# Performance work log

Hardware: AMD Instinct MI355X
Metric: run time of the kernel (lower is better)

Reference implementation:

```python
import jax, jax.numpy as jnp
import numpy as np

B, D, H, E, K = 16384, 4096, 2048, 64, 2
TEMPERATURE = 0.8  # training=True


def setup_inputs() -> dict:
    key = jax.random.key(0)
    k1, k2, k3 = jax.random.split(key, 3)
    x = jax.random.normal(k1, (B, D), dtype=jnp.float32)
    W1 = jax.random.normal(k2, (H, D), dtype=jnp.float32) * 0.02
    b1 = jnp.zeros((H,), dtype=jnp.float32)
    W2 = jax.random.normal(k3, (E, H), dtype=jnp.float32) * 0.02
    b2 = jnp.zeros((E,), dtype=jnp.float32)
    return {"x": x, "W1": W1, "b1": b1, "W2": W2, "b2": b2}


def reference(x, W1, b1, W2, b2):
    # router MLP: Linear(D->H) -> ReLU -> Linear(H->E)
    h = jax.nn.relu(jnp.einsum('bd,hd->bh', x, W1) + b1)
    router_logits = jnp.einsum('bh,eh->be', h, W2) + b2  # [B, E]

    # temperature-scaled softmax for routing
    routing_probs = jax.nn.softmax(router_logits / TEMPERATURE, axis=1)
    routing_weights, expert_indices = jax.lax.top_k(routing_probs, K)  # [B, K]
    routing_weights = routing_weights / routing_weights.sum(axis=1, keepdims=True)

    # entropy-based uncertainty uses UN-scaled logits
    full_probs = jax.nn.softmax(router_logits, axis=1)
    entropy = -jnp.sum(full_probs * jnp.log(full_probs + 1e-10), axis=1).mean()
    uncertainty = entropy / jnp.log(jnp.float32(E))
    return routing_weights, expert_indices, uncertainty
```

## Files before the change

### kernel.cpp

```cpp
#include <hip/hip_runtime.h>
#include <hip/hip_bf16.h>
#include <math.h>

#define B_ROWS 16384
#define D_DIM  4096
#define H_DIM  2048
#define E_DIM  64
#define TEMP   0.8f

typedef __bf16 bf16x8 __attribute__((ext_vector_type(8)));
typedef float  f32x4  __attribute__((ext_vector_type(4)));
typedef unsigned short ushort8 __attribute__((ext_vector_type(8)));

__device__ __forceinline__ unsigned short bf_rne(float f) {
  unsigned u = __float_as_uint(f);
  u += 0x7FFF + ((u >> 16) & 1);
  return (unsigned short)(u >> 16);
}

__device__ __forceinline__ void async_copy16(const void* g, void* l) {
  __builtin_amdgcn_global_load_lds(
      (const __attribute__((address_space(1))) void*)g,
      (__attribute__((address_space(3))) void*)l, 16, 0, 0);
}

__global__ __launch_bounds__(256) void split_kernel(
    const float* __restrict__ in, unsigned short* __restrict__ hi,
    unsigned short* __restrict__ lo) {
  const size_t i = ((size_t)blockIdx.x * 256 + threadIdx.x) * 8;
  float4 v0 = *(const float4*)(in + i);
  float4 v1 = *(const float4*)(in + i + 4);
  float f[8] = {v0.x, v0.y, v0.z, v0.w, v1.x, v1.y, v1.z, v1.w};
  ushort8 hv, lv;
#pragma unroll
  for (int j = 0; j < 8; ++j) {
    unsigned short h = bf_rne(f[j]);
    float fh = __uint_as_float(((unsigned)h) << 16);
    hv[j] = h;
    lv[j] = bf_rne(f[j] - fh);
  }
  *(ushort8*)(hi + i) = hv;
  *(ushort8*)(lo + i) = lv;
}

#define BM 128
#define BN 128
#define BKK 32

__global__ __launch_bounds__(256) void gemm1_mfma_kernel(
    const float* __restrict__ x,
    const unsigned short* __restrict__ w1h,
    const unsigned short* __restrict__ w1l,
    const float* __restrict__ b1, float* __restrict__ Hout) {
  __shared__ unsigned short Ah[BM * BKK];
  __shared__ unsigned short Al[BM * BKK];
  __shared__ unsigned short Bh[BN * BKK];
  __shared__ unsigned short Bl[BN * BKK];

  const int t    = threadIdx.x;
  const int lane = t & 63;
  const int w    = t >> 6;
  const int wm   = w >> 1;
  const int wn   = w & 1;
  const int m0   = blockIdx.y * BM;
  const int n0   = blockIdx.x * BN;

  const int e0 = (w * 2 + 0) * 512 + lane * 8;
  const int e1 = (w * 2 + 1) * 512 + lane * 8;
  const int r0 = e0 >> 5, c0 = e0 & 31;
  const int r1 = e1 >> 5, c1 = e1 & 31;
  const unsigned short* bh_g0 = w1h + (size_t)(n0 + r0) * D_DIM + c0;
  const unsigned short* bh_g1 = w1h + (size_t)(n0 + r1) * D_DIM + c1;
  const unsigned short* bl_g0 = w1l + (size_t)(n0 + r0) * D_DIM + c0;
  const unsigned short* bl_g1 = w1l + (size_t)(n0 + r1) * D_DIM + c1;
  unsigned short* bh_l0 = &Bh[e0];
  unsigned short* bh_l1 = &Bh[e1];
  unsigned short* bl_l0 = &Bl[e0];
  unsigned short* bl_l1 = &Bl[e1];

  const int ar = t >> 1;
  const int ac = (t & 1) * 16;
  const float* xp = x + (size_t)(m0 + ar) * D_DIM + ac;
  unsigned short* ah_w = &Ah[ar * BKK + ac];
  unsigned short* al_w = &Al[ar * BKK + ac];

  const int koff = (lane >> 4) * 8;
  const unsigned short* a_rd[4];
  const unsigned short* b_rd[4];
#pragma unroll
  for (int f = 0; f < 4; ++f) {
    a_rd[f] = &Ah[(wm * 64 + f * 16 + (lane & 15)) * BKK + koff];
    b_rd[f] = &Bh[(wn * 64 + f * 16 + (lane & 15)) * BKK + koff];
  }
  const int lo_off_a = (int)(Al - Ah);
  const int lo_off_b = (int)(Bl - Bh);

  f32x4 acc[4][4];
#pragma unroll
  for (int i = 0; i < 4; ++i)
#pragma unroll
    for (int j = 0; j < 4; ++j) acc[i][j] = (f32x4)0.f;

  for (int k0 = 0; k0 < D_DIM; k0 += BKK) {
    async_copy16(bh_g0 + k0, bh_l0);
    async_copy16(bh_g1 + k0, bh_l1);
    async_copy16(bl_g0 + k0, bl_l0);
    async_copy16(bl_g1 + k0, bl_l1);

    float4 v[4];
#pragma unroll
    for (int j = 0; j < 4; ++j) v[j] = *(const float4*)(xp + k0 + j * 4);
    float f[16] = {v[0].x, v[0].y, v[0].z, v[0].w, v[1].x, v[1].y, v[1].z, v[1].w,
                   v[2].x, v[2].y, v[2].z, v[2].w, v[3].x, v[3].y, v[3].z, v[3].w};
    ushort8 hv0, hv1, lv0, lv1;
#pragma unroll
    for (int j = 0; j < 8; ++j) {
      unsigned short h = bf_rne(f[j]);
      float fh = __uint_as_float(((unsigned)h) << 16);
      hv0[j] = h;
      lv0[j] = bf_rne(f[j] - fh);
    }
#pragma unroll
    for (int j = 0; j < 8; ++j) {
      unsigned short h = bf_rne(f[8 + j]);
      float fh = __uint_as_float(((unsigned)h) << 16);
      hv1[j] = h;
      lv1[j] = bf_rne(f[8 + j] - fh);
    }
    *(ushort8*)(ah_w)     = hv0;
    *(ushort8*)(ah_w + 8) = hv1;
    *(ushort8*)(al_w)     = lv0;
    *(ushort8*)(al_w + 8) = lv1;

    __syncthreads();

    bf16x8 fa_h[4], fa_l[4], fb_h[4], fb_l[4];
#pragma unroll
    for (int ff = 0; ff < 4; ++ff) {
      fa_h[ff] = *(const bf16x8*)(a_rd[ff]);
      fa_l[ff] = *(const bf16x8*)(a_rd[ff] + lo_off_a);
      fb_h[ff] = *(const bf16x8*)(b_rd[ff]);
      fb_l[ff] = *(const bf16x8*)(b_rd[ff] + lo_off_b);
    }
#pragma unroll
    for (int i = 0; i < 4; ++i)
#pragma unroll
      for (int j = 0; j < 4; ++j) {
        acc[i][j] = __builtin_amdgcn_mfma_f32_16x16x32_bf16(fa_h[i], fb_h[j], acc[i][j], 0, 0, 0);
        acc[i][j] = __builtin_amdgcn_mfma_f32_16x16x32_bf16(fa_l[i], fb_h[j], acc[i][j], 0, 0, 0);
        acc[i][j] = __builtin_amdgcn_mfma_f32_16x16x32_bf16(fa_h[i], fb_l[j], acc[i][j], 0, 0, 0);
      }
    __syncthreads();
  }

#pragma unroll
  for (int fn = 0; fn < 4; ++fn) {
    const int n = n0 + wn * 64 + fn * 16 + (lane & 15);
    const float bias = b1[n];
#pragma unroll
    for (int fm = 0; fm < 4; ++fm) {
      const int mbase = m0 + wm * 64 + fm * 16 + (lane >> 4) * 4;
#pragma unroll
      for (int r = 0; r < 4; ++r) {
        float vv = acc[fm][fn][r] + bias;
        Hout[(size_t)(mbase + r) * H_DIM + n] = fmaxf(vv, 0.f);
      }
    }
  }
}

#define F_BM 64
#define F_BK 32

__global__ __launch_bounds__(256) void gemm2_router_kernel(
    const float* __restrict__ h,
    const unsigned short* __restrict__ w2h,
    const unsigned short* __restrict__ w2l,
    const float* __restrict__ b2,
    float* __restrict__ out, float* __restrict__ accum) {
  __shared__ unsigned short Ah[F_BM * F_BK];
  __shared__ unsigned short Al[F_BM * F_BK];
  __shared__ unsigned short Bh[E_DIM * F_BK];
  __shared__ unsigned short Bl[E_DIM * F_BK];
  __shared__ float LG[F_BM][E_DIM + 1];

  const int t    = threadIdx.x;
  const int lane = t & 63;
  const int w    = t >> 6;
  const int m0   = blockIdx.x * F_BM;

  const int ar = t >> 2;
  const int ac = (t & 3) * 8;
  const float* hp = h + (size_t)(m0 + ar) * H_DIM + ac;
  unsigned short* ah_w = &Ah[ar * F_BK + ac];
  unsigned short* al_w = &Al[ar * F_BK + ac];

  const unsigned short* bh_g = w2h + (size_t)ar * H_DIM + ac;
  const unsigned short* bl_g = w2l + (size_t)ar * H_DIM + ac;
  unsigned short* bh_l = &Bh[t * 8];
  unsigned short* bl_l = &Bl[t * 8];

  const int koff = (lane >> 4) * 8;
  const unsigned short* a_rd = &Ah[(w * 16 + (lane & 15)) * F_BK + koff];
  const unsigned short* b_rd[4];
#pragma unroll
  for (int f = 0; f < 4; ++f)
    b_rd[f] = &Bh[(f * 16 + (lane & 15)) * F_BK + koff];
  const int lo_off_a = (int)(Al - Ah);
  const int lo_off_b = (int)(Bl - Bh);

  f32x4 acc[4];
#pragma unroll
  for (int f = 0; f < 4; ++f) acc[f] = (f32x4)0.f;

  for (int k0 = 0; k0 < H_DIM; k0 += F_BK) {
    async_copy16(bh_g + k0, bh_l);
    async_copy16(bl_g + k0, bl_l);

    float4 v0 = *(const float4*)(hp + k0);
    float4 v1 = *(const float4*)(hp + k0 + 4);
    float f[8] = {v0.x, v0.y, v0.z, v0.w, v1.x, v1.y, v1.z, v1.w};
    ushort8 hv, lv;
#pragma unroll
    for (int j = 0; j < 8; ++j) {
      unsigned short hh = bf_rne(f[j]);
      float fh = __uint_as_float(((unsigned)hh) << 16);
      hv[j] = hh;
      lv[j] = bf_rne(f[j] - fh);
    }
    *(ushort8*)ah_w = hv;
    *(ushort8*)al_w = lv;

    __syncthreads();

    bf16x8 fa_h = *(const bf16x8*)(a_rd);
    bf16x8 fa_l = *(const bf16x8*)(a_rd + lo_off_a);
#pragma unroll
    for (int f = 0; f < 4; ++f) {
      bf16x8 fb_h = *(const bf16x8*)(b_rd[f]);
      bf16x8 fb_l = *(const bf16x8*)(b_rd[f] + lo_off_b);
      acc[f] = __builtin_amdgcn_mfma_f32_16x16x32_bf16(fa_h, fb_h, acc[f], 0, 0, 0);
      acc[f] = __builtin_amdgcn_mfma_f32_16x16x32_bf16(fa_l, fb_h, acc[f], 0, 0, 0);
      acc[f] = __builtin_amdgcn_mfma_f32_16x16x32_bf16(fa_h, fb_l, acc[f], 0, 0, 0);
    }
    __syncthreads();
  }

#pragma unroll
  for (int f = 0; f < 4; ++f) {
    const int e = f * 16 + (lane & 15);
    const float bias = b2[e];
#pragma unroll
    for (int r = 0; r < 4; ++r) {
      const int ml = w * 16 + (lane >> 4) * 4 + r;
      LG[ml][e] = acc[f][r] + bias;
    }
  }
  __syncthreads();

  if (t < F_BM) {
    const int row = m0 + t;
    float l0 = LG[t][0]; int i0 = 0;
    float l1 = -INFINITY; int i1 = -1;
#pragma unroll
    for (int e = 1; e < E_DIM; ++e) {
      float v = LG[t][e];
      if (v > l0)      { l1 = l0; i1 = i0; l0 = v; i0 = e; }
      else if (v > l1) { l1 = v; i1 = e; }
    }

    const float eT = expf((l1 - l0) / TEMP);
    const float w0 = 1.f / (1.f + eT);
    const float w1 = eT / (1.f + eT);

    float Z = 0.f;
#pragma unroll
    for (int e = 0; e < E_DIM; ++e) Z += expf(LG[t][e] - l0);
    const float invZ = 1.f / Z;
    float ent = 0.f;
#pragma unroll
    for (int e = 0; e < E_DIM; ++e) {
      float p = expf(LG[t][e] - l0) * invZ;
      ent -= p * logf(p + 1e-10f);
    }

    out[(size_t)row * 2 + 0] = w0;
    out[(size_t)row * 2 + 1] = w1;
    out[(size_t)B_ROWS * 2 + (size_t)row * 2 + 0] = (float)i0;
    out[(size_t)B_ROWS * 2 + (size_t)row * 2 + 1] = (float)i1;

#pragma unroll
    for (int off = 32; off > 0; off >>= 1) ent += __shfl_down(ent, off);
    if (t == 0) atomicAdd(accum, ent);
  }
}

__global__ void zero_kernel(float* p) { p[0] = 0.f; }

__global__ void finalize_kernel(const float* __restrict__ accum,
                                float* __restrict__ out) {
  out[(size_t)B_ROWS * 4] = accum[0] / ((float)B_ROWS * logf((float)E_DIM));
}

extern "C" void kernel_launch(void* const* d_in, const int* in_sizes, int n_in,
                              void* d_out, int out_size, void* d_ws,
                              size_t ws_size, hipStream_t stream) {
  const float* x  = (const float*)d_in[0];
  const float* W1 = (const float*)d_in[1];
  const float* b1 = (const float*)d_in[2];
  const float* W2 = (const float*)d_in[3];
  const float* b2 = (const float*)d_in[4];
  float* out = (float*)d_out;

  unsigned short* w1h = (unsigned short*)d_ws;
  unsigned short* w1l = w1h + (size_t)H_DIM * D_DIM;
  unsigned short* w2h = w1l + (size_t)H_DIM * D_DIM;
  unsigned short* w2l = w2h + (size_t)E_DIM * H_DIM;
  float* h     = (float*)(w2l + (size_t)E_DIM * H_DIM);
  float* accum = h + (size_t)B_ROWS * H_DIM;

  zero_kernel<<<1, 1, 0, stream>>>(accum);

  split_kernel<<<(H_DIM * D_DIM) / (256 * 8), 256, 0, stream>>>(W1, w1h, w1l);
  split_kernel<<<(E_DIM * H_DIM) / (256 * 8), 256, 0, stream>>>(W2, w2h, w2l);

  dim3 g1(H_DIM / BN, B_ROWS / BM);
  gemm1_mfma_kernel<<<g1, 256, 0, stream>>>(x, w1h, w1l, b1, h);

  gemm2_router_kernel<<<B_ROWS / F_BM, 256, 0, stream>>>(h, w2h, w2l, b2, out, accum);

  finalize_kernel<<<1, 1, 0, stream>>>(accum, out);
}
```

Baseline: 1.278 ms.

## Use 32x32 MFMA tiles in GEMM1, deepen and prefetch GEMM2, fold zero kernel

GEMM1 switches from 16x16x32 to 32x32x16 bf16 MFMA instructions with 2x2 fragments per wave, which cuts the LDS fragment reads per MFMA and uses the larger-tile instruction. GEMM2 doubles its K tile to 64 and register-prefetches the next h tile across the barrier, so global latency overlaps with compute and fewer barriers are needed. The accumulator zeroing moves into the W2 split kernel, removing one launch. The costs are higher register pressure from the 16-wide accumulators and more LDS in GEMM2.

```diff
diff --git a/kernel.cpp b/kernel.cpp
--- a/kernel.cpp
+++ b/kernel.cpp
@@ -10,6 +10,7 @@
 
 typedef __bf16 bf16x8 __attribute__((ext_vector_type(8)));
 typedef float  f32x4  __attribute__((ext_vector_type(4)));
+typedef float  f32x16 __attribute__((ext_vector_type(16)));
 typedef unsigned short ushort8 __attribute__((ext_vector_type(8)));
 
 __device__ __forceinline__ unsigned short bf_rne(float f) {
@@ -26,7 +27,8 @@
 
 __global__ __launch_bounds__(256) void split_kernel(
     const float* __restrict__ in, unsigned short* __restrict__ hi,
-    unsigned short* __restrict__ lo) {
+    unsigned short* __restrict__ lo, float* zp) {
+  if (zp && blockIdx.x == 0 && threadIdx.x == 0) *zp = 0.f;
   const size_t i = ((size_t)blockIdx.x * 256 + threadIdx.x) * 8;
   float4 v0 = *(const float4*)(in + i);
   float4 v1 = *(const float4*)(in + i + 4);
@@ -84,22 +86,22 @@
   unsigned short* ah_w = &Ah[ar * BKK + ac];
   unsigned short* al_w = &Al[ar * BKK + ac];
 
-  const int koff = (lane >> 4) * 8;
-  const unsigned short* a_rd[4];
-  const unsigned short* b_rd[4];
-#pragma unroll
-  for (int f = 0; f < 4; ++f) {
-    a_rd[f] = &Ah[(wm * 64 + f * 16 + (lane & 15)) * BKK + koff];
-    b_rd[f] = &Bh[(wn * 64 + f * 16 + (lane & 15)) * BKK + koff];
+  const int koff = (lane >> 5) * 8;
+  const unsigned short* a_rd[2];
+  const unsigned short* b_rd[2];
+#pragma unroll
+  for (int f = 0; f < 2; ++f) {
+    a_rd[f] = &Ah[(wm * 64 + f * 32 + (lane & 31)) * BKK + koff];
+    b_rd[f] = &Bh[(wn * 64 + f * 32 + (lane & 31)) * BKK + koff];
   }
   const int lo_off_a = (int)(Al - Ah);
   const int lo_off_b = (int)(Bl - Bh);
 
-  f32x4 acc[4][4];
-#pragma unroll
-  for (int i = 0; i < 4; ++i)
-#pragma unroll
-    for (int j = 0; j < 4; ++j) acc[i][j] = (f32x4)0.f;
+  f32x16 acc[2][2];
+#pragma unroll
+  for (int i = 0; i < 2; ++i)
+#pragma unroll
+    for (int j = 0; j < 2; ++j) acc[i][j] = (f32x16)0.f;
 
   for (int k0 = 0; k0 < D_DIM; k0 += BKK) {
     async_copy16(bh_g0 + k0, bh_l0);
@@ -134,43 +136,48 @@
 
     __syncthreads();
 
-    bf16x8 fa_h[4], fa_l[4], fb_h[4], fb_l[4];
-#pragma unroll
-    for (int ff = 0; ff < 4; ++ff) {
-      fa_h[ff] = *(const bf16x8*)(a_rd[ff]);
-      fa_l[ff] = *(const bf16x8*)(a_rd[ff] + lo_off_a);
-      fb_h[ff] = *(const bf16x8*)(b_rd[ff]);
-      fb_l[ff] = *(const bf16x8*)(b_rd[ff] + lo_off_b);
-    }
-#pragma unroll
-    for (int i = 0; i < 4; ++i)
-#pragma unroll
-      for (int j = 0; j < 4; ++j) {
-        acc[i][j] = __builtin_amdgcn_mfma_f32_16x16x32_bf16(fa_h[i], fb_h[j], acc[i][j], 0, 0, 0);
-        acc[i][j] = __builtin_amdgcn_mfma_f32_16x16x32_bf16(fa_l[i], fb_h[j], acc[i][j], 0, 0, 0);
-        acc[i][j] = __builtin_amdgcn_mfma_f32_16x16x32_bf16(fa_h[i], fb_l[j], acc[i][j], 0, 0, 0);
+#pragma unroll
+    for (int ks = 0; ks < 2; ++ks) {
+      const int ko = ks * 16;
+      bf16x8 fa_h[2], fa_l[2], fb_h[2], fb_l[2];
+#pragma unroll
+      for (int ff = 0; ff < 2; ++ff) {
+        fa_h[ff] = *(const bf16x8*)(a_rd[ff] + ko);
+        fa_l[ff] = *(const bf16x8*)(a_rd[ff] + ko + lo_off_a);
+        fb_h[ff] = *(const bf16x8*)(b_rd[ff] + ko);
+        fb_l[ff] = *(const bf16x8*)(b_rd[ff] + ko + lo_off_b);
       }
+#pragma unroll
+      for (int i = 0; i < 2; ++i)
+#pragma unroll
+        for (int j = 0; j < 2; ++j) {
+          acc[i][j] = __builtin_amdgcn_mfma_f32_32x32x16_bf16(fa_h[i], fb_h[j], acc[i][j], 0, 0, 0);
+          acc[i][j] = __builtin_amdgcn_mfma_f32_32x32x16_bf16(fa_l[i], fb_h[j], acc[i][j], 0, 0, 0);
+          acc[i][j] = __builtin_amdgcn_mfma_f32_32x32x16_bf16(fa_h[i], fb_l[j], acc[i][j], 0, 0, 0);
+        }
+    }
     __syncthreads();
   }
 
 #pragma unroll
-  for (int fn = 0; fn < 4; ++fn) {
-    const int n = n0 + wn * 64 + fn * 16 + (lane & 15);
+  for (int fn = 0; fn < 2; ++fn) {
+    const int n = n0 + wn * 64 + fn * 32 + (lane & 31);
     const float bias = b1[n];
 #pragma unroll
-    for (int fm = 0; fm < 4; ++fm) {
-      const int mbase = m0 + wm * 64 + fm * 16 + (lane >> 4) * 4;
-#pragma unroll
-      for (int r = 0; r < 4; ++r) {
-        float vv = acc[fm][fn][r] + bias;
-        Hout[(size_t)(mbase + r) * H_DIM + n] = fmaxf(vv, 0.f);
+    for (int fm = 0; fm < 2; ++fm) {
+      const int mbase = m0 + wm * 64 + fm * 32 + 4 * (lane >> 5);
+#pragma unroll
+      for (int reg = 0; reg < 16; ++reg) {
+        const int row = mbase + (reg & 3) + 8 * (reg >> 2);
+        float vv = acc[fm][fn][reg] + bias;
+        Hout[(size_t)row * H_DIM + n] = fmaxf(vv, 0.f);
       }
     }
   }
 }
 
 #define F_BM 64
-#define F_BK 32
+#define F_BK 64
 
 __global__ __launch_bounds__(256) void gemm2_router_kernel(
     const float* __restrict__ h,
@@ -190,15 +197,23 @@
   const int m0   = blockIdx.x * F_BM;
 
   const int ar = t >> 2;
-  const int ac = (t & 3) * 8;
+  const int ac = (t & 3) * 16;
   const float* hp = h + (size_t)(m0 + ar) * H_DIM + ac;
   unsigned short* ah_w = &Ah[ar * F_BK + ac];
   unsigned short* al_w = &Al[ar * F_BK + ac];
 
-  const unsigned short* bh_g = w2h + (size_t)ar * H_DIM + ac;
-  const unsigned short* bl_g = w2l + (size_t)ar * H_DIM + ac;
-  unsigned short* bh_l = &Bh[t * 8];
-  unsigned short* bl_l = &Bl[t * 8];
+  const int e0 = (w * 2 + 0) * 512 + lane * 8;
+  const int e1 = (w * 2 + 1) * 512 + lane * 8;
+  const int r0 = e0 >> 6, c0 = e0 & 63;
+  const int r1 = e1 >> 6, c1 = e1 & 63;
+  const unsigned short* bh_g0 = w2h + (size_t)r0 * H_DIM + c0;
+  const unsigned short* bh_g1 = w2h + (size_t)r1 * H_DIM + c1;
+  const unsigned short* bl_g0 = w2l + (size_t)r0 * H_DIM + c0;
+  const unsigned short* bl_g1 = w2l + (size_t)r1 * H_DIM + c1;
+  unsigned short* bh_l0 = &Bh[e0];
+  unsigned short* bh_l1 = &Bh[e1];
+  unsigned short* bl_l0 = &Bl[e0];
+  unsigned short* bl_l1 = &Bl[e1];
 
   const int koff = (lane >> 4) * 8;
   const unsigned short* a_rd = &Ah[(w * 16 + (lane & 15)) * F_BK + koff];
@@ -213,35 +228,62 @@
 #pragma unroll
   for (int f = 0; f < 4; ++f) acc[f] = (f32x4)0.f;
 
+  float4 p0 = *(const float4*)(hp);
+  float4 p1 = *(const float4*)(hp + 4);
+  float4 p2 = *(const float4*)(hp + 8);
+  float4 p3 = *(const float4*)(hp + 12);
+
   for (int k0 = 0; k0 < H_DIM; k0 += F_BK) {
-    async_copy16(bh_g + k0, bh_l);
-    async_copy16(bl_g + k0, bl_l);
-
-    float4 v0 = *(const float4*)(hp + k0);
-    float4 v1 = *(const float4*)(hp + k0 + 4);
-    float f[8] = {v0.x, v0.y, v0.z, v0.w, v1.x, v1.y, v1.z, v1.w};
-    ushort8 hv, lv;
+    float f[16] = {p0.x, p0.y, p0.z, p0.w, p1.x, p1.y, p1.z, p1.w,
+                   p2.x, p2.y, p2.z, p2.w, p3.x, p3.y, p3.z, p3.w};
+    ushort8 hv0, hv1, lv0, lv1;
 #pragma unroll
     for (int j = 0; j < 8; ++j) {
       unsigned short hh = bf_rne(f[j]);
       float fh = __uint_as_float(((unsigned)hh) << 16);
-      hv[j] = hh;
-      lv[j] = bf_rne(f[j] - fh);
-    }
-    *(ushort8*)ah_w = hv;
-    *(ushort8*)al_w = lv;
+      hv0[j] = hh;
+      lv0[j] = bf_rne(f[j] - fh);
+    }
+#pragma unroll
+    for (int j = 0; j < 8; ++j) {
+      unsigned short hh = bf_rne(f[8 + j]);
+      float fh = __uint_as_float(((unsigned)hh) << 16);
+      hv1[j] = hh;
+      lv1[j] = bf_rne(f[8 + j] - fh);
+    }
+    *(ushort8*)(ah_w)     = hv0;
+    *(ushort8*)(ah_w + 8) = hv1;
+    *(ushort8*)(al_w)     = lv0;
+    *(ushort8*)(al_w + 8) = lv1;
+
+    async_copy16(bh_g0 + k0, bh_l0);
+    async_copy16(bh_g1 + k0, bh_l1);
+    async_copy16(bl_g0 + k0, bl_l0);
+    async_copy16(bl_g1 + k0, bl_l1);
 
     __syncthreads();
 
-    bf16x8 fa_h = *(const bf16x8*)(a_rd);
-    bf16x8 fa_l = *(const bf16x8*)(a_rd + lo_off_a);
-#pragma unroll
-    for (int f = 0; f < 4; ++f) {
-      bf16x8 fb_h = *(const bf16x8*)(b_rd[f]);
-      bf16x8 fb_l = *(const bf16x8*)(b_rd[f] + lo_off_b);
-      acc[f] = __builtin_amdgcn_mfma_f32_16x16x32_bf16(fa_h, fb_h, acc[f], 0, 0, 0);
-      acc[f] = __builtin_amdgcn_mfma_f32_16x16x32_bf16(fa_l, fb_h, acc[f], 0, 0, 0);
-      acc[f] = __builtin_amdgcn_mfma_f32_16x16x32_bf16(fa_h, fb_l, acc[f], 0, 0, 0);
+    if (k0 + F_BK < H_DIM) {
+      const float* hpn = hp + k0 + F_BK;
+      p0 = *(const float4*)(hpn);
+      p1 = *(const float4*)(hpn + 4);
+      p2 = *(const float4*)(hpn + 8);
+      p3 = *(const float4*)(hpn + 12);
+    }
+
+#pragma unroll
+    for (int ks = 0; ks < 2; ++ks) {
+      const int ko = ks * 32;
+      bf16x8 fa_h = *(const bf16x8*)(a_rd + ko);
+      bf16x8 fa_l = *(const bf16x8*)(a_rd + ko + lo_off_a);
+#pragma unroll
+      for (int f = 0; f < 4; ++f) {
+        bf16x8 fb_h = *(const bf16x8*)(b_rd[f] + ko);
+        bf16x8 fb_l = *(const bf16x8*)(b_rd[f] + ko + lo_off_b);
+        acc[f] = __builtin_amdgcn_mfma_f32_16x16x32_bf16(fa_h, fb_h, acc[f], 0, 0, 0);
+        acc[f] = __builtin_amdgcn_mfma_f32_16x16x32_bf16(fa_l, fb_h, acc[f], 0, 0, 0);
+        acc[f] = __builtin_amdgcn_mfma_f32_16x16x32_bf16(fa_h, fb_l, acc[f], 0, 0, 0);
+      }
     }
     __syncthreads();
   }
@@ -294,8 +336,6 @@
     if (t == 0) atomicAdd(accum, ent);
   }
 }
-
-__global__ void zero_kernel(float* p) { p[0] = 0.f; }
 
 __global__ void finalize_kernel(const float* __restrict__ accum,
                                 float* __restrict__ out) {
@@ -319,10 +359,8 @@
   float* h     = (float*)(w2l + (size_t)E_DIM * H_DIM);
   float* accum = h + (size_t)B_ROWS * H_DIM;
 
-  zero_kernel<<<1, 1, 0, stream>>>(accum);
-
-  split_kernel<<<(H_DIM * D_DIM) / (256 * 8), 256, 0, stream>>>(W1, w1h, w1l);
-  split_kernel<<<(E_DIM * H_DIM) / (256 * 8), 256, 0, stream>>>(W2, w2h, w2l);
+  split_kernel<<<(H_DIM * D_DIM) / (256 * 8), 256, 0, stream>>>(W1, w1h, w1l, nullptr);
+  split_kernel<<<(E_DIM * H_DIM) / (256 * 8), 256, 0, stream>>>(W2, w2h, w2l, accum);
 
   dim3 g1(H_DIM / BN, B_ROWS / BM);
   gemm1_mfma_kernel<<<g1, 256, 0, stream>>>(x, w1h, w1l, b1, h);
```

Measured after the change: 1.344 ms. 5.2% more time.
